# Performance work log

Measured on AMD Instinct MI355X. Metric: run time of the kernel, lower is better.

The kernel has to match this reference:

```python
import jax, jax.numpy as jnp
import numpy as np

B, N, D, H, L = 2, 2048, 512, 8, 2
HD = D // H


def setup_inputs() -> dict:
    key = jax.random.key(0)
    ks = jax.random.split(key, 8)
    s = 0.02
    return {
        "inputs_embeds": jax.random.normal(ks[0], (B, N, D), jnp.float32),
        "pos_emb": jax.random.normal(ks[1], (N, D), jnp.float32) * s,
        "c_attn_w": jax.random.normal(ks[2], (L, D, 3 * D), jnp.float32) * s,
        "c_attn_b": jnp.zeros((L, 3 * D), jnp.float32),
        "out_w": jax.random.normal(ks[3], (L, D, D), jnp.float32) * s,
        "out_b": jnp.zeros((L, D), jnp.float32),
        "ln1_g": jnp.ones((L, D), jnp.float32),
        "ln1_b": jnp.zeros((L, D), jnp.float32),
        "c_fc_w": jax.random.normal(ks[4], (L, D, 4 * D), jnp.float32) * s,
        "c_fc_b": jnp.zeros((L, 4 * D), jnp.float32),
        "c_proj_w": jax.random.normal(ks[5], (L, 4 * D, D), jnp.float32) * s,
        "c_proj_b": jnp.zeros((L, D), jnp.float32),
        "ln2_g": jnp.ones((L, D), jnp.float32),
        "ln2_b": jnp.zeros((L, D), jnp.float32),
    }


def _layernorm(x, g, b, eps=1e-5):
    mu = jnp.mean(x, axis=-1, keepdims=True)
    var = jnp.mean(jnp.square(x - mu), axis=-1, keepdims=True)
    return (x - mu) * jax.lax.rsqrt(var + eps) * g + b


def _gelu_new(x):
    # NewGELUActivation: tanh approximation
    return 0.5 * x * (1.0 + jnp.tanh(jnp.sqrt(2.0 / jnp.pi) * (x + 0.044715 * x ** 3)))


def _attention(x, w_qkv, b_qkv, w_out, b_out, self_mask):
    qkv = x @ w_qkv + b_qkv                      # [B,N,3D]
    q, k, v = jnp.split(qkv, 3, axis=-1)
    def heads(t):
        return t.reshape(B, N, H, HD).transpose(0, 2, 1, 3)  # [B,H,N,HD]
    q, k, v = heads(q), heads(k), heads(v)
    scores = jnp.einsum('bhqd,bhkd->bhqk', q, k) / jnp.sqrt(jnp.float32(HD))
    neg = jnp.finfo(scores.dtype).min
    scores = jnp.where(self_mask, scores, neg)   # exclude-self mask
    attn = jax.nn.softmax(scores, axis=-1)
    o = jnp.einsum('bhqk,bhkd->bhqd', attn, v)
    o = o.transpose(0, 2, 1, 3).reshape(B, N, D)
    return o @ w_out + b_out


def reference(inputs_embeds, pos_emb, c_attn_w, c_attn_b, out_w, out_b,
              ln1_g, ln1_b, c_fc_w, c_fc_b, c_proj_w, c_proj_b, ln2_g, ln2_b):
    self_mask = ~jnp.eye(N, dtype=bool)[None, None]  # [1,1,N,N]
    h = inputs_embeds + pos_emb[None]
    for l in range(L):
        res = h
        x = _layernorm(h, ln1_g[l], ln1_b[l])
        h = _attention(x, c_attn_w[l], c_attn_b[l], out_w[l], out_b[l], self_mask) + res
        res = h
        x = _layernorm(h, ln2_g[l], ln2_b[l])
        x = _gelu_new(x @ c_fc_w[l] + c_fc_b[l])
        h = (x @ c_proj_w[l] + c_proj_b[l]) + res
    return h
```

## Files before the change

kernel.cpp:

```cpp
#include <hip/hip_runtime.h>
#include <hip/hip_bf16.h>
#include <math.h>

#define BB 2
#define NN 2048
#define DD 512
#define HH 8
#define LL 2
#define TT (BB*NN)

typedef short short8 __attribute__((ext_vector_type(8)));
typedef float floatx4 __attribute__((ext_vector_type(4)));

__device__ __forceinline__ unsigned short f2b(float v) {
    union { float f; unsigned u; } x; x.f = v;
    unsigned r = x.u + 0x7fff + ((x.u >> 16) & 1);
    return (unsigned short)(r >> 16);
}

__global__ __launch_bounds__(256) void k_bias_add(const float* __restrict__ src,
                                                  const float* __restrict__ bias,
                                                  float* __restrict__ dst) {
    int i = blockIdx.x * 256 + threadIdx.x;
    dst[i] = src[i] + bias[i & (DD - 1)];
}

template <int EMB>
__global__ __launch_bounds__(256) void k_ln(const float* __restrict__ hin,
                                            unsigned short* __restrict__ xout,
                                            const float* __restrict__ g,
                                            const float* __restrict__ b,
                                            const float* __restrict__ emb,
                                            const float* __restrict__ pos,
                                            float* __restrict__ hout) {
    __shared__ float red[4];
    __shared__ float bc1, bc2;
    int t = blockIdx.x;
    int tid = threadIdx.x;
    int lane = tid & 63, wv = tid >> 6;
    float v0, v1;
    if (EMB) {
        const float* erow = emb + (size_t)t * DD;
        const float* prow = pos + (size_t)(t & (NN - 1)) * DD;
        v0 = erow[tid] + prow[tid];
        v1 = erow[tid + 256] + prow[tid + 256];
        hout[(size_t)t * DD + tid] = v0;
        hout[(size_t)t * DD + tid + 256] = v1;
    } else {
        const float* row = hin + (size_t)t * DD;
        v0 = row[tid];
        v1 = row[tid + 256];
    }

    float s = v0 + v1;
#pragma unroll
    for (int o = 32; o; o >>= 1) s += __shfl_down(s, o, 64);
    if (lane == 0) red[wv] = s;
    __syncthreads();
    if (tid == 0) bc1 = (red[0] + red[1] + red[2] + red[3]) * (1.0f / DD);
    __syncthreads();
    float mu = bc1;
    float d0 = v0 - mu, d1 = v1 - mu;
    s = d0 * d0 + d1 * d1;
#pragma unroll
    for (int o = 32; o; o >>= 1) s += __shfl_down(s, o, 64);
    if (lane == 0) red[wv] = s;
    __syncthreads();
    if (tid == 0) bc2 = (red[0] + red[1] + red[2] + red[3]) * (1.0f / DD);
    __syncthreads();
    float rstd = rsqrtf(bc2 + 1e-5f);
    xout[(size_t)t * DD + tid]       = f2b(d0 * rstd * g[tid] + b[tid]);
    xout[(size_t)t * DD + tid + 256] = f2b(d1 * rstd * g[tid + 256] + b[tid + 256]);
}

__device__ __forceinline__ float gelu_new(float v) {
    const float c = 0.7978845608028654f;
    float u = c * (v + 0.044715f * v * v * v);
    return 0.5f * v * (1.0f + tanhf(u));
}

#define PL 3145728
__global__ __launch_bounds__(256) void k_wt_all(const float* __restrict__ c_attn_w,
                                                const float* __restrict__ out_w,
                                                const float* __restrict__ c_fc_w,
                                                const float* __restrict__ c_proj_w,
                                                unsigned short* __restrict__ wbuf) {
    __shared__ unsigned short t[64][72];
    int bx = blockIdx.x;
    int l = bx / 768;
    int r = bx - l * 768;
    const float* W; unsigned short* WT; int K, N;
    if (r < 192)      { W = c_attn_w + (size_t)l * 512 * 1536; WT = wbuf + (size_t)l * PL;           K = 512;  N = 1536; }
    else if (r < 256) { r -= 192; W = out_w  + (size_t)l * 512 * 512;  WT = wbuf + (size_t)l * PL + 786432;  K = 512;  N = 512; }
    else if (r < 512) { r -= 256; W = c_fc_w + (size_t)l * 512 * 2048; WT = wbuf + (size_t)l * PL + 1048576; K = 512;  N = 2048; }
    else              { r -= 512; W = c_proj_w + (size_t)l * 2048 * 512; WT = wbuf + (size_t)l * PL + 2097152; K = 2048; N = 512; }
    int tiles_n = N >> 6;
    int n0 = (r % tiles_n) * 64, k0 = (r / tiles_n) * 64;

    int tid = threadIdx.x;
    int rr = tid >> 2;
    int c0 = (tid & 3) * 16;
    const float* src = W + (size_t)(k0 + rr) * N + n0 + c0;
#pragma unroll
    for (int u = 0; u < 4; u++) {
        float4 v = *(const float4*)&src[u * 4];
        t[c0 + u * 4 + 0][rr] = f2b(v.x);
        t[c0 + u * 4 + 1][rr] = f2b(v.y);
        t[c0 + u * 4 + 2][rr] = f2b(v.z);
        t[c0 + u * 4 + 3][rr] = f2b(v.w);
    }
    __syncthreads();
    unsigned short* dst = WT + (size_t)(n0 + rr) * K + k0 + c0;
#pragma unroll
    for (int u = 0; u < 4; u++)
        *(uint2*)&dst[u * 4] = *(const uint2*)&t[rr][c0 + u * 4];
}

template <int ACT, int BF16OUT, int ATOMIC>
__global__ __launch_bounds__(256) void k_mgemm(const unsigned short* __restrict__ Ab,
                                               const unsigned short* __restrict__ Bt,
                                               const float* __restrict__ bias,
                                               float* __restrict__ Cp,
                                               unsigned short* __restrict__ Cb,
                                               int Kfull, int Kchunk, int N) {
    __shared__ unsigned short Als[2][8 * 512];
    __shared__ unsigned short Bls[2][8 * 512];

    int tid = threadIdx.x;
    int l = tid & 63, w = tid >> 6;
    int wm = w >> 1, wn = w & 1;
    int m0 = blockIdx.y * 128, n0 = blockIdx.x * 128;
    int kb = blockIdx.z * Kchunk;
    int lr = l & 15;
    int lk = (l >> 4) * 8;

    const unsigned short* Ap0 = Ab + (size_t)(m0 + (w * 2 + 0) * 16 + lr) * Kfull + kb + lk;
    const unsigned short* Ap1 = Ab + (size_t)(m0 + (w * 2 + 1) * 16 + lr) * Kfull + kb + lk;
    const unsigned short* Bp0 = Bt + (size_t)(n0 + (w * 2 + 0) * 16 + lr) * Kfull + kb + lk;
    const unsigned short* Bp1 = Bt + (size_t)(n0 + (w * 2 + 1) * 16 + lr) * Kfull + kb + lk;
    int la0 = (w * 2 + 0) * 512 + l * 8;
    int la1 = (w * 2 + 1) * 512 + l * 8;

    floatx4 acc[4][4];
#pragma unroll
    for (int i = 0; i < 4; i++)
#pragma unroll
        for (int j = 0; j < 4; j++) acc[i][j] = (floatx4){0.f, 0.f, 0.f, 0.f};

    int nit = Kchunk >> 5;

    uint4 ra0 = *(const uint4*)Ap0;
    uint4 ra1 = *(const uint4*)Ap1;
    uint4 rb0 = *(const uint4*)Bp0;
    uint4 rb1 = *(const uint4*)Bp1;
    *(uint4*)&Als[0][la0] = ra0;
    *(uint4*)&Als[0][la1] = ra1;
    *(uint4*)&Bls[0][la0] = rb0;
    *(uint4*)&Bls[0][la1] = rb1;
    if (nit > 1) {
        ra0 = *(const uint4*)(Ap0 + 32);
        ra1 = *(const uint4*)(Ap1 + 32);
        rb0 = *(const uint4*)(Bp0 + 32);
        rb1 = *(const uint4*)(Bp1 + 32);
    }
    __syncthreads();

    for (int it = 0; it < nit; it++) {
        int c = it & 1;
        if (it + 1 < nit) {
            *(uint4*)&Als[c ^ 1][la0] = ra0;
            *(uint4*)&Als[c ^ 1][la1] = ra1;
            *(uint4*)&Bls[c ^ 1][la0] = rb0;
            *(uint4*)&Bls[c ^ 1][la1] = rb1;
        }
        if (it + 2 < nit) {
            int ko = (it + 2) << 5;
            ra0 = *(const uint4*)(Ap0 + ko);
            ra1 = *(const uint4*)(Ap1 + ko);
            rb0 = *(const uint4*)(Bp0 + ko);
            rb1 = *(const uint4*)(Bp1 + ko);
        }
        short8 a[4], b[4];
#pragma unroll
        for (int i = 0; i < 4; i++) {
            a[i] = *(const short8*)&Als[c][(wm * 4 + i) * 512 + l * 8];
            b[i] = *(const short8*)&Bls[c][(wn * 4 + i) * 512 + l * 8];
        }
#pragma unroll
        for (int i = 0; i < 4; i++)
#pragma unroll
            for (int j = 0; j < 4; j++)
                acc[i][j] = __builtin_amdgcn_mfma_f32_16x16x32_bf16(a[i], b[j], acc[i][j], 0, 0, 0);
        __syncthreads();
    }

    int col_in = l & 15, rquad = (l >> 4) * 4;
    bool addb = (!ATOMIC) || (bias != nullptr && blockIdx.z == 0);
#pragma unroll
    for (int i = 0; i < 4; i++) {
        int gm_base = m0 + wm * 64 + i * 16 + rquad;
#pragma unroll
        for (int j = 0; j < 4; j++) {
            int gn = n0 + wn * 64 + j * 16 + col_in;
            float bv = addb ? bias[gn] : 0.0f;
#pragma unroll
            for (int r = 0; r < 4; r++) {
                size_t off = (size_t)(gm_base + r) * N + gn;
                if (ATOMIC) {
                    atomicAdd(&Cp[off], acc[i][j][r] + bv);
                } else {
                    float v = acc[i][j][r] + bv;
                    if (ACT) v = gelu_new(v);
                    if (BF16OUT) Cb[off] = f2b(v);
                    else Cp[off] = v;
                }
            }
        }
    }
}

__global__ __launch_bounds__(256) void k_attn_mfma(const unsigned short* __restrict__ qkv,
                                                   unsigned short* __restrict__ xatt) {
    __shared__ unsigned short Ks[64 * 72];
    __shared__ unsigned short Vt[64 * 72];
    __shared__ unsigned short Pls[64 * 72];

    int qt = blockIdx.x, hd = blockIdx.y, b = blockIdx.z;
    int tid = threadIdx.x;
    int l = tid & 63, w = tid >> 6;
    int lr = l & 15, quad = l >> 4;

    const size_t base = (size_t)b * NN * 1536;

    short8 qf[2];
    {
        const unsigned short* qrow = qkv + base + (size_t)(qt * 64 + w * 16 + lr) * 1536 + hd * 64;
        qf[0] = *(const short8*)&qrow[quad * 8];
        qf[1] = *(const short8*)&qrow[quad * 8 + 32];
    }

    floatx4 O[4];
#pragma unroll
    for (int jd = 0; jd < 4; jd++) O[jd] = (floatx4){0.f, 0.f, 0.f, 0.f};
    float lsum = 0.0f;

    int sr = tid >> 2, sc = (tid & 3) * 16;
    int vk = (tid & 15) * 4, vd = (tid >> 4) * 4;
    const unsigned short* Kbase = qkv + base + 512 + hd * 64;
    const unsigned short* Vbase = qkv + base + 1024 + hd * 64;

    uint4 rk0, rk1;
    union { uint2 u; unsigned short s[4]; } rv[4];
    rk0 = *(const uint4*)&Kbase[(size_t)sr * 1536 + sc];
    rk1 = *(const uint4*)&Kbase[(size_t)sr * 1536 + sc + 8];
#pragma unroll
    for (int i = 0; i < 4; i++)
        rv[i].u = *(const uint2*)&Vbase[(size_t)(vk + i) * 1536 + vd];

    const float EC1 = 0.18033688011112042f;
    const float EC0 = -11.541560327111707f;

    for (int kt = 0; kt < 32; kt++) {
        __syncthreads();
        *(uint4*)&Ks[sr * 72 + sc]     = rk0;
        *(uint4*)&Ks[sr * 72 + sc + 8] = rk1;
#pragma unroll
        for (int j = 0; j < 4; j++) {
            union { uint2 u; unsigned short s[4]; } pk;
            pk.s[0] = rv[0].s[j]; pk.s[1] = rv[1].s[j];
            pk.s[2] = rv[2].s[j]; pk.s[3] = rv[3].s[j];
            *(uint2*)&Vt[(vd + j) * 72 + vk] = pk.u;
        }
        __syncthreads();
        if (kt < 31) {
            int kn = (kt + 1) * 64;
            rk0 = *(const uint4*)&Kbase[(size_t)(kn + sr) * 1536 + sc];
            rk1 = *(const uint4*)&Kbase[(size_t)(kn + sr) * 1536 + sc + 8];
#pragma unroll
            for (int i = 0; i < 4; i++)
                rv[i].u = *(const uint2*)&Vbase[(size_t)(kn + vk + i) * 1536 + vd];
        }

        floatx4 s[4];
#pragma unroll
        for (int jn = 0; jn < 4; jn++) s[jn] = (floatx4){0.f, 0.f, 0.f, 0.f};
#pragma unroll
        for (int ss = 0; ss < 2; ss++)
#pragma unroll
            for (int jn = 0; jn < 4; jn++) {
                short8 ak = *(const short8*)&Ks[(jn * 16 + lr) * 72 + ss * 32 + quad * 8];
                s[jn] = __builtin_amdgcn_mfma_f32_16x16x32_bf16(ak, qf[ss], s[jn], 0, 0, 0);
            }

        int mq = w * 16 + lr;
        bool diag = (kt == qt);
#pragma unroll
        for (int jn = 0; jn < 4; jn++) {
            float p0 = __builtin_amdgcn_exp2f(fmaf(s[jn][0], EC1, EC0));
            float p1 = __builtin_amdgcn_exp2f(fmaf(s[jn][1], EC1, EC0));
            float p2 = __builtin_amdgcn_exp2f(fmaf(s[jn][2], EC1, EC0));
            float p3 = __builtin_amdgcn_exp2f(fmaf(s[jn][3], EC1, EC0));
            if (diag) {
                int kbase = jn * 16 + quad * 4;
                if (mq == kbase + 0) p0 = 0.0f;
                if (mq == kbase + 1) p1 = 0.0f;
                if (mq == kbase + 2) p2 = 0.0f;
                if (mq == kbase + 3) p3 = 0.0f;
            }
            lsum += (p0 + p1) + (p2 + p3);
            unsigned w01, w23;
            asm("v_cvt_pk_bf16_f32 %0, %1, %2" : "=v"(w01) : "v"(p0), "v"(p1));
            asm("v_cvt_pk_bf16_f32 %0, %1, %2" : "=v"(w23) : "v"(p2), "v"(p3));
            uint2 pku; pku.x = w01; pku.y = w23;
            *(uint2*)&Pls[mq * 72 + jn * 16 + quad * 4] = pku;
        }

#pragma unroll
        for (int ss = 0; ss < 2; ss++) {
            short8 ap = *(const short8*)&Pls[(w * 16 + lr) * 72 + ss * 32 + quad * 8];
#pragma unroll
            for (int jd = 0; jd < 4; jd++) {
                short8 bv = *(const short8*)&Vt[(jd * 16 + lr) * 72 + ss * 32 + quad * 8];
                O[jd] = __builtin_amdgcn_mfma_f32_16x16x32_bf16(ap, bv, O[jd], 0, 0, 0);
            }
        }
    }

    lsum += __shfl_xor(lsum, 16);
    lsum += __shfl_xor(lsum, 32);
#pragma unroll
    for (int r = 0; r < 4; r++) {
        float inv = 1.0f / __shfl(lsum, quad * 4 + r, 16);
        size_t tok = (size_t)b * NN + qt * 64 + w * 16 + quad * 4 + r;
#pragma unroll
        for (int jd = 0; jd < 4; jd++)
            xatt[tok * DD + hd * 64 + jd * 16 + lr] = f2b(O[jd][r] * inv);
    }
}

extern "C" void kernel_launch(void* const* d_in, const int* in_sizes, int n_in,
                              void* d_out, int out_size, void* d_ws, size_t ws_size,
                              hipStream_t stream) {
    const float* emb      = (const float*)d_in[0];
    const float* pos      = (const float*)d_in[1];
    const float* c_attn_w = (const float*)d_in[2];
    const float* c_attn_b = (const float*)d_in[3];
    const float* out_w    = (const float*)d_in[4];
    const float* out_b    = (const float*)d_in[5];
    const float* ln1_g    = (const float*)d_in[6];
    const float* ln1_b    = (const float*)d_in[7];
    const float* c_fc_w   = (const float*)d_in[8];
    const float* c_fc_b   = (const float*)d_in[9];
    const float* c_proj_w = (const float*)d_in[10];
    const float* c_proj_b = (const float*)d_in[11];
    const float* ln2_g    = (const float*)d_in[12];
    const float* ln2_b    = (const float*)d_in[13];

    char* p = (char*)d_ws;
    float* h = (float*)p;                       p += (size_t)TT * DD * 4;
    unsigned short* act = (unsigned short*)p;   p += (size_t)TT * 2048 * 2;
    unsigned short* x = (unsigned short*)p;     p += (size_t)TT * DD * 2;
    unsigned short* xatt = (unsigned short*)p;  p += (size_t)TT * DD * 2;
    unsigned short* wbuf = (unsigned short*)p;

    unsigned short* qkvb = act;
    unsigned short* ffa  = act;
    float* out = (float*)d_out;

    k_wt_all<<<1536, 256, 0, stream>>>(c_attn_w, out_w, c_fc_w, c_proj_w, wbuf);

    for (int l = 0; l < LL; l++) {
        unsigned short* wqkv_t  = wbuf + (size_t)l * PL;
        unsigned short* wout_t  = wqkv_t + 786432;
        unsigned short* wfc_t   = wqkv_t + 1048576;
        unsigned short* wproj_t = wqkv_t + 2097152;

        if (l == 0)
            k_ln<1><<<TT, 256, 0, stream>>>(nullptr, x, ln1_g, ln1_b, emb, pos, h);
        else
            k_ln<0><<<TT, 256, 0, stream>>>(h, x, ln1_g + l * DD, ln1_b + l * DD,
                                            nullptr, nullptr, nullptr);
        k_mgemm<0, 1, 0><<<dim3(1536 / 128, TT / 128), 256, 0, stream>>>(
            x, wqkv_t, c_attn_b + l * 1536, nullptr, qkvb, 512, 512, 1536);
        k_attn_mfma<<<dim3(NN / 64, HH, BB), 256, 0, stream>>>(qkvb, xatt);
        k_mgemm<0, 0, 1><<<dim3(512 / 128, TT / 128, 2), 256, 0, stream>>>(
            xatt, wout_t, out_b + l * DD, h, nullptr, 512, 256, 512);
        k_ln<0><<<TT, 256, 0, stream>>>(h, x, ln2_g + l * DD, ln2_b + l * DD,
                                        nullptr, nullptr, nullptr);
        k_mgemm<1, 1, 0><<<dim3(2048 / 128, TT / 128), 256, 0, stream>>>(
            x, wfc_t, c_fc_b + l * 2048, nullptr, ffa, 512, 512, 2048);
        if (l == LL - 1) {
            k_bias_add<<<TT * DD / 256, 256, 0, stream>>>(h, c_proj_b + l * DD, out);
            k_mgemm<0, 0, 1><<<dim3(512 / 128, TT / 128, 4), 256, 0, stream>>>(
                ffa, wproj_t, nullptr, out, nullptr, 2048, 512, 512);
        } else {
            k_mgemm<0, 0, 1><<<dim3(512 / 128, TT / 128, 4), 256, 0, stream>>>(
                ffa, wproj_t, c_proj_b + l * DD, h, nullptr, 2048, 512, 512);
        }
    }
}
```

Measured before the change: 427.8 us.

## Split attention over key range with combine kernel; raise split-K for projections

Attention is split into two key-range halves per query tile, doubling the grid. Each half writes unnormalized fp32 partial outputs and row sums, and a new combine kernel sums them and normalizes to bf16. The out-projection and FC-proj GEMMs use more split-K slices with atomic accumulation. This adds a launch, extra fp32 traffic and more atomics in exchange for better occupancy. The combine has no max rescaling, so it relies on the softmax using a fixed exponent offset rather than a running max.

```diff
diff --git a/kernel.cpp b/kernel.cpp
--- a/kernel.cpp
+++ b/kernel.cpp
@@ -220,17 +220,20 @@
 }
 
 __global__ __launch_bounds__(256) void k_attn_mfma(const unsigned short* __restrict__ qkv,
-                                                   unsigned short* __restrict__ xatt) {
+                                                   float* __restrict__ Opart,
+                                                   float* __restrict__ Lpart) {
     __shared__ unsigned short Ks[64 * 72];
     __shared__ unsigned short Vt[64 * 72];
     __shared__ unsigned short Pls[64 * 72];
 
-    int qt = blockIdx.x, hd = blockIdx.y, b = blockIdx.z;
+    int qt = blockIdx.x, hd = blockIdx.y;
+    int b = blockIdx.z >> 1, ck = blockIdx.z & 1;
     int tid = threadIdx.x;
     int l = tid & 63, w = tid >> 6;
     int lr = l & 15, quad = l >> 4;
 
     const size_t base = (size_t)b * NN * 1536;
+    const int k0 = ck * 16, k1 = k0 + 16;
 
     short8 qf[2];
     {
@@ -251,16 +254,19 @@
 
     uint4 rk0, rk1;
     union { uint2 u; unsigned short s[4]; } rv[4];
-    rk0 = *(const uint4*)&Kbase[(size_t)sr * 1536 + sc];
-    rk1 = *(const uint4*)&Kbase[(size_t)sr * 1536 + sc + 8];
-#pragma unroll
-    for (int i = 0; i < 4; i++)
-        rv[i].u = *(const uint2*)&Vbase[(size_t)(vk + i) * 1536 + vd];
+    {
+        int kn = k0 * 64;
+        rk0 = *(const uint4*)&Kbase[(size_t)(kn + sr) * 1536 + sc];
+        rk1 = *(const uint4*)&Kbase[(size_t)(kn + sr) * 1536 + sc + 8];
+#pragma unroll
+        for (int i = 0; i < 4; i++)
+            rv[i].u = *(const uint2*)&Vbase[(size_t)(kn + vk + i) * 1536 + vd];
+    }
 
     const float EC1 = 0.18033688011112042f;
     const float EC0 = -11.541560327111707f;
 
-    for (int kt = 0; kt < 32; kt++) {
+    for (int kt = k0; kt < k1; kt++) {
         __syncthreads();
         *(uint4*)&Ks[sr * 72 + sc]     = rk0;
         *(uint4*)&Ks[sr * 72 + sc + 8] = rk1;
@@ -272,7 +278,7 @@
             *(uint2*)&Vt[(vd + j) * 72 + vk] = pk.u;
         }
         __syncthreads();
-        if (kt < 31) {
+        if (kt + 1 < k1) {
             int kn = (kt + 1) * 64;
             rk0 = *(const uint4*)&Kbase[(size_t)(kn + sr) * 1536 + sc];
             rk1 = *(const uint4*)&Kbase[(size_t)(kn + sr) * 1536 + sc + 8];
@@ -328,14 +334,34 @@
 
     lsum += __shfl_xor(lsum, 16);
     lsum += __shfl_xor(lsum, 32);
+
+    float* Op = Opart + (size_t)ck * TT * DD;
+    float* Lp = Lpart + (size_t)ck * TT * HH;
+    if (quad == 0)
+        Lp[(size_t)(b * NN + qt * 64 + w * 16 + lr) * HH + hd] = lsum;
 #pragma unroll
     for (int r = 0; r < 4; r++) {
-        float inv = 1.0f / __shfl(lsum, quad * 4 + r, 16);
         size_t tok = (size_t)b * NN + qt * 64 + w * 16 + quad * 4 + r;
 #pragma unroll
         for (int jd = 0; jd < 4; jd++)
-            xatt[tok * DD + hd * 64 + jd * 16 + lr] = f2b(O[jd][r] * inv);
-    }
+            Op[tok * DD + hd * 64 + jd * 16 + lr] = O[jd][r];
+    }
+}
+
+__global__ __launch_bounds__(256) void k_att_combine(const float* __restrict__ Opart,
+                                                     const float* __restrict__ Lpart,
+                                                     unsigned short* __restrict__ xatt) {
+    int tok = blockIdx.x, tid = threadIdx.x;
+    const float* O0 = Opart;
+    const float* O1 = Opart + (size_t)TT * DD;
+    const float* L0 = Lpart;
+    const float* L1 = Lpart + (size_t)TT * HH;
+    size_t o = (size_t)tok * DD;
+    int d0 = tid, d1 = tid + 256;
+    float ia = 1.0f / (L0[(size_t)tok * HH + (d0 >> 6)] + L1[(size_t)tok * HH + (d0 >> 6)]);
+    float ib = 1.0f / (L0[(size_t)tok * HH + (d1 >> 6)] + L1[(size_t)tok * HH + (d1 >> 6)]);
+    xatt[o + d0] = f2b((O0[o + d0] + O1[o + d0]) * ia);
+    xatt[o + d1] = f2b((O0[o + d1] + O1[o + d1]) * ib);
 }
 
 extern "C" void kernel_launch(void* const* d_in, const int* in_sizes, int n_in,
@@ -347,21 +373,27 @@
     const float* c_attn_b = (const float*)d_in[3];
     const float* out_w    = (const float*)d_in[4];
     const float* out_b    = (const float*)d_in[5];
+    const float* c_fc_w   = (const float*)d_in[6 - 2];
+    const float* dummy    = nullptr; (void)dummy;
+    const float* out_b_   = out_b; (void)out_b_;
     const float* ln1_g    = (const float*)d_in[6];
     const float* ln1_b    = (const float*)d_in[7];
-    const float* c_fc_w   = (const float*)d_in[8];
+    const float* c_fc_w2  = (const float*)d_in[8];
     const float* c_fc_b   = (const float*)d_in[9];
     const float* c_proj_w = (const float*)d_in[10];
     const float* c_proj_b = (const float*)d_in[11];
     const float* ln2_g    = (const float*)d_in[12];
     const float* ln2_b    = (const float*)d_in[13];
+    c_fc_w = c_fc_w2;
 
     char* p = (char*)d_ws;
     float* h = (float*)p;                       p += (size_t)TT * DD * 4;
     unsigned short* act = (unsigned short*)p;   p += (size_t)TT * 2048 * 2;
     unsigned short* x = (unsigned short*)p;     p += (size_t)TT * DD * 2;
     unsigned short* xatt = (unsigned short*)p;  p += (size_t)TT * DD * 2;
-    unsigned short* wbuf = (unsigned short*)p;
+    unsigned short* wbuf = (unsigned short*)p;  p += (size_t)2 * PL * 2;
+    float* Opart = (float*)p;                   p += (size_t)2 * TT * DD * 4;
+    float* Lpart = (float*)p;                   p += (size_t)2 * TT * HH * 4;
 
     unsigned short* qkvb = act;
     unsigned short* ffa  = act;
@@ -382,20 +414,21 @@
                                             nullptr, nullptr, nullptr);
         k_mgemm<0, 1, 0><<<dim3(1536 / 128, TT / 128), 256, 0, stream>>>(
             x, wqkv_t, c_attn_b + l * 1536, nullptr, qkvb, 512, 512, 1536);
-        k_attn_mfma<<<dim3(NN / 64, HH, BB), 256, 0, stream>>>(qkvb, xatt);
-        k_mgemm<0, 0, 1><<<dim3(512 / 128, TT / 128, 2), 256, 0, stream>>>(
-            xatt, wout_t, out_b + l * DD, h, nullptr, 512, 256, 512);
+        k_attn_mfma<<<dim3(NN / 64, HH, BB * 2), 256, 0, stream>>>(qkvb, Opart, Lpart);
+        k_att_combine<<<TT, 256, 0, stream>>>(Opart, Lpart, xatt);
+        k_mgemm<0, 0, 1><<<dim3(512 / 128, TT / 128, 4), 256, 0, stream>>>(
+            xatt, wout_t, out_b + l * DD, h, nullptr, 512, 128, 512);
         k_ln<0><<<TT, 256, 0, stream>>>(h, x, ln2_g + l * DD, ln2_b + l * DD,
                                         nullptr, nullptr, nullptr);
         k_mgemm<1, 1, 0><<<dim3(2048 / 128, TT / 128), 256, 0, stream>>>(
             x, wfc_t, c_fc_b + l * 2048, nullptr, ffa, 512, 512, 2048);
         if (l == LL - 1) {
             k_bias_add<<<TT * DD / 256, 256, 0, stream>>>(h, c_proj_b + l * DD, out);
-            k_mgemm<0, 0, 1><<<dim3(512 / 128, TT / 128, 4), 256, 0, stream>>>(
-                ffa, wproj_t, nullptr, out, nullptr, 2048, 512, 512);
+            k_mgemm<0, 0, 1><<<dim3(512 / 128, TT / 128, 8), 256, 0, stream>>>(
+                ffa, wproj_t, nullptr, out, nullptr, 2048, 256, 512);
         } else {
-            k_mgemm<0, 0, 1><<<dim3(512 / 128, TT / 128, 4), 256, 0, stream>>>(
-                ffa, wproj_t, c_proj_b + l * DD, h, nullptr, 2048, 512, 512);
-        }
-    }
-}
+            k_mgemm<0, 0, 1><<<dim3(512 / 128, TT / 128, 8), 256, 0, stream>>>(
+                ffa, wproj_t, c_proj_b + l * DD, h, nullptr, 2048, 256, 512);
+        }
+    }
+}
```

New measurement: 525.3 us. +22.8%, slower.

## Use 512-thread GEMM blocks with 4x2 warp grid and fast exp-based GELU

Applied to the files above, without the earlier changes.

The GEMM kernel now runs 8 waves per 128x128 tile instead of 4. Each wave computes a 64x32 sub-tile, and each thread does one global load per operand per k-step. This halves the accumulators per thread, aiming for more latency hiding and occupancy. It costs more waves sharing the same LDS tile and more redundant A-fragment reads. Separately, GELU's tanhf is replaced by a clamped exp2/rcp sigmoid form, cutting transcendental cost in the FC epilogue at some small accuracy loss.

```diff
diff --git a/kernel.cpp b/kernel.cpp
--- a/kernel.cpp
+++ b/kernel.cpp
@@ -76,7 +76,9 @@
 __device__ __forceinline__ float gelu_new(float v) {
     const float c = 0.7978845608028654f;
     float u = c * (v + 0.044715f * v * v * v);
-    return 0.5f * v * (1.0f + tanhf(u));
+    u = fminf(fmaxf(u, -30.0f), 30.0f);
+    float e = __builtin_amdgcn_exp2f(2.885390081777927f * u);
+    return v * e * __builtin_amdgcn_rcpf(e + 1.0f);
 }
 
 #define PL 3145728
@@ -117,7 +119,7 @@
 }
 
 template <int ACT, int BF16OUT, int ATOMIC>
-__global__ __launch_bounds__(256) void k_mgemm(const unsigned short* __restrict__ Ab,
+__global__ __launch_bounds__(512) void k_mgemm(const unsigned short* __restrict__ Ab,
                                                const unsigned short* __restrict__ Bt,
                                                const float* __restrict__ bias,
                                                float* __restrict__ Cp,
@@ -128,68 +130,56 @@
 
     int tid = threadIdx.x;
     int l = tid & 63, w = tid >> 6;
-    int wm = w >> 1, wn = w & 1;
+    int wm = w >> 2, wn = w & 3;
     int m0 = blockIdx.y * 128, n0 = blockIdx.x * 128;
     int kb = blockIdx.z * Kchunk;
     int lr = l & 15;
     int lk = (l >> 4) * 8;
 
-    const unsigned short* Ap0 = Ab + (size_t)(m0 + (w * 2 + 0) * 16 + lr) * Kfull + kb + lk;
-    const unsigned short* Ap1 = Ab + (size_t)(m0 + (w * 2 + 1) * 16 + lr) * Kfull + kb + lk;
-    const unsigned short* Bp0 = Bt + (size_t)(n0 + (w * 2 + 0) * 16 + lr) * Kfull + kb + lk;
-    const unsigned short* Bp1 = Bt + (size_t)(n0 + (w * 2 + 1) * 16 + lr) * Kfull + kb + lk;
-    int la0 = (w * 2 + 0) * 512 + l * 8;
-    int la1 = (w * 2 + 1) * 512 + l * 8;
-
-    floatx4 acc[4][4];
+    const unsigned short* Ap = Ab + (size_t)(m0 + w * 16 + lr) * Kfull + kb + lk;
+    const unsigned short* Bp = Bt + (size_t)(n0 + w * 16 + lr) * Kfull + kb + lk;
+    int la = w * 512 + l * 8;
+
+    floatx4 acc[4][2];
 #pragma unroll
     for (int i = 0; i < 4; i++)
 #pragma unroll
-        for (int j = 0; j < 4; j++) acc[i][j] = (floatx4){0.f, 0.f, 0.f, 0.f};
+        for (int j = 0; j < 2; j++) acc[i][j] = (floatx4){0.f, 0.f, 0.f, 0.f};
 
     int nit = Kchunk >> 5;
 
-    uint4 ra0 = *(const uint4*)Ap0;
-    uint4 ra1 = *(const uint4*)Ap1;
-    uint4 rb0 = *(const uint4*)Bp0;
-    uint4 rb1 = *(const uint4*)Bp1;
-    *(uint4*)&Als[0][la0] = ra0;
-    *(uint4*)&Als[0][la1] = ra1;
-    *(uint4*)&Bls[0][la0] = rb0;
-    *(uint4*)&Bls[0][la1] = rb1;
+    uint4 ra = *(const uint4*)Ap;
+    uint4 rb = *(const uint4*)Bp;
+    *(uint4*)&Als[0][la] = ra;
+    *(uint4*)&Bls[0][la] = rb;
     if (nit > 1) {
-        ra0 = *(const uint4*)(Ap0 + 32);
-        ra1 = *(const uint4*)(Ap1 + 32);
-        rb0 = *(const uint4*)(Bp0 + 32);
-        rb1 = *(const uint4*)(Bp1 + 32);
+        ra = *(const uint4*)(Ap + 32);
+        rb = *(const uint4*)(Bp + 32);
     }
     __syncthreads();
 
     for (int it = 0; it < nit; it++) {
         int c = it & 1;
         if (it + 1 < nit) {
-            *(uint4*)&Als[c ^ 1][la0] = ra0;
-            *(uint4*)&Als[c ^ 1][la1] = ra1;
-            *(uint4*)&Bls[c ^ 1][la0] = rb0;
-            *(uint4*)&Bls[c ^ 1][la1] = rb1;
+            *(uint4*)&Als[c ^ 1][la] = ra;
+            *(uint4*)&Bls[c ^ 1][la] = rb;
         }
         if (it + 2 < nit) {
             int ko = (it + 2) << 5;
-            ra0 = *(const uint4*)(Ap0 + ko);
-            ra1 = *(const uint4*)(Ap1 + ko);
-            rb0 = *(const uint4*)(Bp0 + ko);
-            rb1 = *(const uint4*)(Bp1 + ko);
-        }
-        short8 a[4], b[4];
-#pragma unroll
-        for (int i = 0; i < 4; i++) {
+            ra = *(const uint4*)(Ap + ko);
+            rb = *(const uint4*)(Bp + ko);
+        }
+        short8 a[4], b[2];
+#pragma unroll
+        for (int i = 0; i < 4; i++)
             a[i] = *(const short8*)&Als[c][(wm * 4 + i) * 512 + l * 8];
-            b[i] = *(const short8*)&Bls[c][(wn * 4 + i) * 512 + l * 8];
-        }
+#pragma unroll
+        for (int j = 0; j < 2; j++)
+            b[j] = *(const short8*)&Bls[c][(wn * 2 + j) * 512 + l * 8];
 #pragma unroll
         for (int i = 0; i < 4; i++)
 #pragma unroll
-            for (int j = 0; j < 4; j++)
+            for (int j = 0; j < 2; j++)
                 acc[i][j] = __builtin_amdgcn_mfma_f32_16x16x32_bf16(a[i], b[j], acc[i][j], 0, 0, 0);
         __syncthreads();
     }
@@ -200,8 +190,8 @@
     for (int i = 0; i < 4; i++) {
         int gm_base = m0 + wm * 64 + i * 16 + rquad;
 #pragma unroll
-        for (int j = 0; j < 4; j++) {
-            int gn = n0 + wn * 64 + j * 16 + col_in;
+        for (int j = 0; j < 2; j++) {
+            int gn = n0 + wn * 32 + j * 16 + col_in;
             float bv = addb ? bias[gn] : 0.0f;
 #pragma unroll
             for (int r = 0; r < 4; r++) {
@@ -380,21 +370,21 @@
         else
             k_ln<0><<<TT, 256, 0, stream>>>(h, x, ln1_g + l * DD, ln1_b + l * DD,
                                             nullptr, nullptr, nullptr);
-        k_mgemm<0, 1, 0><<<dim3(1536 / 128, TT / 128), 256, 0, stream>>>(
+        k_mgemm<0, 1, 0><<<dim3(1536 / 128, TT / 128), 512, 0, stream>>>(
             x, wqkv_t, c_attn_b + l * 1536, nullptr, qkvb, 512, 512, 1536);
         k_attn_mfma<<<dim3(NN / 64, HH, BB), 256, 0, stream>>>(qkvb, xatt);
-        k_mgemm<0, 0, 1><<<dim3(512 / 128, TT / 128, 2), 256, 0, stream>>>(
+        k_mgemm<0, 0, 1><<<dim3(512 / 128, TT / 128, 2), 512, 0, stream>>>(
             xatt, wout_t, out_b + l * DD, h, nullptr, 512, 256, 512);
         k_ln<0><<<TT, 256, 0, stream>>>(h, x, ln2_g + l * DD, ln2_b + l * DD,
                                         nullptr, nullptr, nullptr);
-        k_mgemm<1, 1, 0><<<dim3(2048 / 128, TT / 128), 256, 0, stream>>>(
+        k_mgemm<1, 1, 0><<<dim3(2048 / 128, TT / 128), 512, 0, stream>>>(
             x, wfc_t, c_fc_b + l * 2048, nullptr, ffa, 512, 512, 2048);
         if (l == LL - 1) {
             k_bias_add<<<TT * DD / 256, 256, 0, stream>>>(h, c_proj_b + l * DD, out);
-            k_mgemm<0, 0, 1><<<dim3(512 / 128, TT / 128, 4), 256, 0, stream>>>(
+            k_mgemm<0, 0, 1><<<dim3(512 / 128, TT / 128, 4), 512, 0, stream>>>(
                 ffa, wproj_t, nullptr, out, nullptr, 2048, 512, 512);
         } else {
-            k_mgemm<0, 0, 1><<<dim3(512 / 128, TT / 128, 4), 256, 0, stream>>>(
+            k_mgemm<0, 0, 1><<<dim3(512 / 128, TT / 128, 4), 512, 0, stream>>>(
                 ffa, wproj_t, c_proj_b + l * DD, h, nullptr, 2048, 512, 512);
         }
     }
```

Measured after the change: 415.8 us. 2.8% less time.
